# Kernel optimization log

Measured on AMD Instinct MI355X. Metric: run time of the kernel, lower is better.

The kernel has to match this reference:

```python
import jax, jax.numpy as jnp
import numpy as np

NUM_HEADS = 8
HEAD_DIM = 64  # d_model 512 / 8 heads


def rope(x):
    # x: (B, S, D). Rotary applied over the FULL hidden dim (as in source),
    # with even/odd halves CONCATENATED (not interleaved) on output.
    b, s, d = x.shape
    pos = jnp.arange(s, dtype=jnp.float32)[:, None]                      # (S, 1)
    freqs = jnp.exp(jnp.arange(0, d, 2, dtype=jnp.float32) * (-np.log(10000.0) / d))  # (D/2,)
    ang = pos * freqs                                                     # (S, D/2)
    cos = jnp.cos(ang)[None, :, :]
    sin = jnp.sin(ang)[None, :, :]
    xe = x[..., 0::2]
    xo = x[..., 1::2]
    return jnp.concatenate([xe * cos - xo * sin, xo * cos + xe * sin], axis=-1)


def split_heads(x):
    b, s, d = x.shape
    return x.reshape(b, s, NUM_HEADS, HEAD_DIM).transpose(0, 2, 1, 3)  # (B,H,S,hd)


def setup_inputs() -> dict:
    key = jax.random.key(0)
    ks = jax.random.split(key, 8)
    B, S, D = 2, 2048, 512
    sc = 1.0 / np.sqrt(D)
    return {
        "querys": jax.random.normal(ks[0], (B, S, D), jnp.float32),
        "keys": jax.random.normal(ks[1], (B, S, D), jnp.float32),
        "values": jax.random.normal(ks[2], (B, S, D), jnp.float32),
        "attn_mask": jnp.zeros((B, 1, S, S), jnp.float32),
        "Wq": jax.random.normal(ks[3], (D, D), jnp.float32) * sc,
        "Wk": jax.random.normal(ks[4], (D, D), jnp.float32) * sc,
        "Wv": jax.random.normal(ks[5], (D, D), jnp.float32) * sc,
        "Wo": jax.random.normal(ks[6], (D, D), jnp.float32) * sc,
    }


def reference(querys, keys, values, attn_mask, Wq, Wk, Wv, Wo):
    q = split_heads(rope(querys @ Wq.T))   # (B,H,Sq,hd)
    k = split_heads(rope(keys @ Wk.T))     # (B,H,Sk,hd)
    v = split_heads(values @ Wv.T)         # (B,H,Sk,hd)

    logits = jnp.einsum("bhqd,bhkd->bhqk", q, k)
    # mask added BEFORE scaling, exactly as in the source
    logits = logits + attn_mask[:, :, : q.shape[2], : k.shape[2]] * (-1e9)
    attn_scores = jax.nn.softmax(logits / np.float32(HEAD_DIM) ** 0.5, axis=-1)

    embeds = jnp.einsum("bhqk,bhkd->bhqd", attn_scores, v)
    b, h, s, hd = embeds.shape
    embeds = embeds.transpose(0, 2, 1, 3).reshape(b, s, h * hd) @ Wo.T
    return embeds, attn_scores
```

## Files before the change

### kernel.cpp

```cpp
#include <hip/hip_runtime.h>
#include <hip/hip_fp16.h>

typedef _Float16 f16x8 __attribute__((ext_vector_type(8)));
typedef _Float16 f16x4 __attribute__((ext_vector_type(4)));
typedef float f32x16 __attribute__((ext_vector_type(16)));
typedef float f32x4 __attribute__((ext_vector_type(4)));

#define LOG2E 1.44269504088896340736f
#define QSCALE 0.18033688011112042f
#define MASKC 1.8033688e8f

typedef __attribute__((address_space(1))) const unsigned char gl_byte;
typedef __attribute__((address_space(3))) unsigned char lds_byte;

#define GLOAD_LDS16(g, l) \
  __builtin_amdgcn_global_load_lds((const gl_byte*)(g), (lds_byte*)(l), 16, 0, 0)

static __device__ __forceinline__ f32x16 zero16() {
  f32x16 z;
#pragma unroll
  for (int i = 0; i < 16; ++i) z[i] = 0.0f;
  return z;
}

static __device__ __forceinline__ unsigned pkh(float a, float b) {
  union { _Float16 h[2]; unsigned u; } t;
  t.h[0] = (_Float16)a; t.h[1] = (_Float16)b;
  return t.u;
}

static __device__ __forceinline__ void swap32(unsigned x, unsigned y, int hi,
                                              unsigned& a, unsigned& c) {
  unsigned py = (unsigned)__shfl_xor((int)y, 32);
  unsigned px = (unsigned)__shfl_xor((int)x, 32);
  a = hi ? py : x;
  c = hi ? y : px;
}

static __device__ __forceinline__ void stage_k64(char* dst,
                                                 const _Float16* __restrict__ kr,
                                                 int b, int h, int kb, int tid) {
#pragma unroll
  for (int it = 0; it < 4; ++it) {
    int s = it * 128 + tid;
    int r = s >> 3, c8 = (s & 7) ^ (r & 7);
    const _Float16* g = kr + (size_t)(b * 2048 + kb * 64 + r) * 512 + h * 64 + c8 * 8;
    GLOAD_LDS16(g, dst + (it * 128 + (tid & 64)) * 16);
  }
}

__global__ __launch_bounds__(256) void proj_kernel(
    const float* __restrict__ qin, const float* __restrict__ kin,
    const float* __restrict__ vin, const float* __restrict__ Wq,
    const float* __restrict__ Wk, const float* __restrict__ Wv,
    const float* __restrict__ mask, int* __restrict__ flag,
    _Float16* __restrict__ q_r, _Float16* __restrict__ k_r,
    _Float16* __restrict__ v_t) {
  __shared__ char smem[8192 + 16384];
  const int tid = threadIdx.x;
  const int zz = blockIdx.z;

  if (zz == 3) {
    int bid = blockIdx.y * 4 + blockIdx.x;
    const float4* m4p = (const float4*)mask;
    int base = bid * 8192 + tid;
    bool nz = false;
#pragma unroll 4
    for (int i = 0; i < 32; ++i) {
      float4 v = m4p[base + i * 256];
      nz |= (v.x != 0.f) || (v.y != 0.f) || (v.z != 0.f) || (v.w != 0.f);
    }
    if (__any(nz) && (tid & 63) == 0) atomicOr(flag, 1);
    return;
  }

  const int l = tid & 63, lo = l & 31, hi = l >> 5;
  const int w = tid >> 6, wm = w >> 1, wn = w & 1;
  const int m0 = blockIdx.y * 64, n0 = blockIdx.x * 128;
  const float* A = zz == 0 ? qin : zz == 1 ? kin : vin;
  const float* W = zz == 0 ? Wq : zz == 1 ? Wk : Wv;

  f32x16 acc[2];
  acc[0] = zero16();
  acc[1] = zero16();

  for (int kb = 0; kb < 8; ++kb) {
#pragma unroll
    for (int i = 0; i < 4; ++i) {
      int idx = tid + 256 * i; int r = idx >> 4, c4 = idx & 15;
      float4 v = *(const float4*)(A + (size_t)(m0 + r) * 512 + kb * 64 + c4 * 4);
      uint2 uu; uu.x = pkh(v.x, v.y); uu.y = pkh(v.z, v.w);
      *(uint2*)(smem + ((r * 128 + c4 * 8) ^ ((r & 7) << 4))) = uu;
    }
#pragma unroll
    for (int i = 0; i < 8; ++i) {
      int idx = tid + 256 * i; int r = idx >> 4, c4 = idx & 15;
      float4 v = *(const float4*)(W + (size_t)(n0 + r) * 512 + kb * 64 + c4 * 4);
      uint2 uu; uu.x = pkh(v.x, v.y); uu.y = pkh(v.z, v.w);
      *(uint2*)(smem + 8192 + ((r * 128 + c4 * 8) ^ ((r & 7) << 4))) = uu;
    }
    __syncthreads();
#pragma unroll
    for (int ks = 0; ks < 4; ++ks) {
      int ra = wm * 32 + lo;
      f16x8 a0 = *(const f16x8*)(smem + ((ra * 128 + ks * 32 + hi * 16) ^ ((ra & 7) << 4)));
      int rb0 = wn * 64 + lo, rb1 = rb0 + 32;
      f16x8 b0 = *(const f16x8*)(smem + 8192 + ((rb0 * 128 + ks * 32 + hi * 16) ^ ((rb0 & 7) << 4)));
      f16x8 b1 = *(const f16x8*)(smem + 8192 + ((rb1 * 128 + ks * 32 + hi * 16) ^ ((rb1 & 7) << 4)));
      acc[0] = __builtin_amdgcn_mfma_f32_32x32x16_f16(a0, b0, acc[0], 0, 0, 0);
      acc[1] = __builtin_amdgcn_mfma_f32_32x32x16_f16(a0, b1, acc[1], 0, 0, 0);
    }
    __syncthreads();
  }

  if (zz < 2) {
    _Float16* out = zz ? k_r : q_r;
#pragma unroll
    for (int nt = 0; nt < 2; ++nt) {
      int n = n0 + wn * 64 + nt * 32 + lo;
      int odd = lo & 1;
      int ii = (n >> 1) & 255;
      float fr = exp2f(-(float)ii * 0.05190512648261504f);
#pragma unroll
      for (int r = 0; r < 16; ++r) {
        int m = m0 + wm * 32 + (r & 3) + 8 * ((r >> 2) & 3) + 4 * hi;
        float a = acc[nt][r];
        float bb = __shfl_xor(a, 1);
        float xe = odd ? bb : a, xo = odd ? a : bb;
        float ang = (float)(m & 2047) * fr;
        float sn, cs;
        sincosf(ang, &sn, &cs);
        float res = odd ? (xo * cs + xe * sn) : (xe * cs - xo * sn);
        if (zz == 0) res *= QSCALE;
        out[(size_t)m * 512 + ii + (odd ? 256 : 0)] = (_Float16)res;
      }
    }
  } else {
#pragma unroll
    for (int nt = 0; nt < 2; ++nt) {
      int n = n0 + wn * 64 + nt * 32 + lo;
      int hh = n >> 6, d = n & 63;
#pragma unroll
      for (int a = 0; a < 4; ++a) {
        int m = m0 + wm * 32 + 8 * a + 4 * hi;
        int b_ = m >> 11, s = m & 2047;
        uint2 uu;
        uu.x = pkh(acc[nt][4 * a + 0], acc[nt][4 * a + 1]);
        uu.y = pkh(acc[nt][4 * a + 2], acc[nt][4 * a + 3]);
        *(uint2*)(v_t + (size_t)((b_ * 8 + hh) * 64 + d) * 2048 + s) = uu;
      }
    }
  }
}

__global__ __launch_bounds__(256) void out_gemm(const _Float16* __restrict__ opart,
                                                const float* __restrict__ W,
                                                float* __restrict__ out) {
  __shared__ char smem[8192 + 16384];
  const int tid = threadIdx.x;
  const int l = tid & 63, lo = l & 31, hi = l >> 5;
  const int w = tid >> 6, wm = w >> 1, wn = w & 1;
  const int m0 = blockIdx.y * 64, n0 = blockIdx.x * 128;
  const size_t slab = (size_t)4096 * 512;

  f32x16 acc[2];
  acc[0] = zero16();
  acc[1] = zero16();

  for (int kb = 0; kb < 8; ++kb) {
#pragma unroll
    for (int i = 0; i < 4; ++i) {
      int idx = tid + 256 * i; int r = idx >> 4, c4 = idx & 15;
      size_t off = (size_t)(m0 + r) * 512 + kb * 64 + c4 * 4;
      f16x4 x = *(const f16x4*)(opart + off);
      f16x4 y = *(const f16x4*)(opart + slab + off);
      f16x4 u = *(const f16x4*)(opart + 2 * slab + off);
      f16x4 t = *(const f16x4*)(opart + 3 * slab + off);
      float s0 = (float)x[0] + (float)y[0] + (float)u[0] + (float)t[0];
      float s1 = (float)x[1] + (float)y[1] + (float)u[1] + (float)t[1];
      float s2 = (float)x[2] + (float)y[2] + (float)u[2] + (float)t[2];
      float s3 = (float)x[3] + (float)y[3] + (float)u[3] + (float)t[3];
      uint2 uu; uu.x = pkh(s0, s1); uu.y = pkh(s2, s3);
      *(uint2*)(smem + ((r * 128 + c4 * 8) ^ ((r & 7) << 4))) = uu;
    }
#pragma unroll
    for (int i = 0; i < 8; ++i) {
      int idx = tid + 256 * i; int r = idx >> 4, c4 = idx & 15;
      float4 v = *(const float4*)(W + (size_t)(n0 + r) * 512 + kb * 64 + c4 * 4);
      uint2 uu; uu.x = pkh(v.x, v.y); uu.y = pkh(v.z, v.w);
      *(uint2*)(smem + 8192 + ((r * 128 + c4 * 8) ^ ((r & 7) << 4))) = uu;
    }
    __syncthreads();
#pragma unroll
    for (int ks = 0; ks < 4; ++ks) {
      int ra = wm * 32 + lo;
      f16x8 a0 = *(const f16x8*)(smem + ((ra * 128 + ks * 32 + hi * 16) ^ ((ra & 7) << 4)));
      int rb0 = wn * 64 + lo, rb1 = rb0 + 32;
      f16x8 b0 = *(const f16x8*)(smem + 8192 + ((rb0 * 128 + ks * 32 + hi * 16) ^ ((rb0 & 7) << 4)));
      f16x8 b1 = *(const f16x8*)(smem + 8192 + ((rb1 * 128 + ks * 32 + hi * 16) ^ ((rb1 & 7) << 4)));
      acc[0] = __builtin_amdgcn_mfma_f32_32x32x16_f16(a0, b0, acc[0], 0, 0, 0);
      acc[1] = __builtin_amdgcn_mfma_f32_32x32x16_f16(a0, b1, acc[1], 0, 0, 0);
    }
    __syncthreads();
  }

#pragma unroll
  for (int nt = 0; nt < 2; ++nt) {
    int n = n0 + wn * 64 + nt * 32 + lo;
#pragma unroll
    for (int r = 0; r < 16; ++r) {
      int m = m0 + wm * 32 + (r & 3) + 8 * ((r >> 2) & 3) + 4 * hi;
      out[(size_t)m * 512 + n] = acc[nt][r];
    }
  }
}

__global__ __launch_bounds__(128, 4) void lsum_kernel(
    const _Float16* __restrict__ qr, const _Float16* __restrict__ kr,
    const float* __restrict__ mask, const int* __restrict__ flagp,
    float* __restrict__ lsums) {
  __shared__ char smem[16384];
  const int tid = threadIdx.x;
  const int w = tid >> 6, l = tid & 63, lo = l & 31, hi = l >> 5;
  const int bh = blockIdx.y, b = bh >> 3, h = bh & 7;
  const int q0 = blockIdx.x * 64, z = blockIdx.z;
  const int mflag = *flagp;
  const int qw = q0 + w * 32 + lo;

  f16x8 qf[4];
  {
    const _Float16* qrow = qr + (size_t)(b * 2048 + qw) * 512 + h * 64 + hi * 8;
#pragma unroll
    for (int ks = 0; ks < 4; ++ks) qf[ks] = *(const f16x8*)(qrow + ks * 16);
  }

  const int kb0 = z * 8;
  stage_k64(smem, kr, b, h, kb0, tid);
  __syncthreads();

  float lsum = 0.f;
  for (int t = 0; t < 8; ++t) {
    const int cur = t & 1, kb = kb0 + t;
    if (t < 7) stage_k64(smem + (cur ^ 1) * 8192, kr, b, h, kb + 1, tid);
    char* kbuf = smem + cur * 8192;
#pragma unroll
    for (int ks4 = 0; ks4 < 2; ++ks4) {
      f32x16 acc = zero16();
      int krw = ks4 * 32 + lo;
#pragma unroll
      for (int ks = 0; ks < 4; ++ks) {
        f16x8 kf = *(const f16x8*)(kbuf + ((krw * 128 + ks * 32 + hi * 16) ^ ((krw & 7) << 4)));
        acc = __builtin_amdgcn_mfma_f32_32x32x16_f16(kf, qf[ks], acc, 0, 0, 0);
      }
      if (!mflag) {
#pragma unroll
        for (int r = 0; r < 16; ++r) lsum += exp2f(acc[r]);
      } else {
#pragma unroll
        for (int r = 0; r < 16; ++r) {
          int kg = kb * 64 + ks4 * 32 + (r & 3) + 8 * ((r >> 2) & 3) + 4 * hi;
          float mv = mask[(size_t)(b * 2048 + qw) * 2048 + kg];
          lsum += exp2f(acc[r] - MASKC * mv);
        }
      }
    }
    __syncthreads();
  }
  lsum += __shfl_xor(lsum, 32);
  if (hi == 0) lsums[(size_t)(z * 16 + bh) * 2048 + qw] = lsum;
}

__global__ __launch_bounds__(128, 4) void attn_kernel(
    const _Float16* __restrict__ qr, const _Float16* __restrict__ kr,
    const _Float16* __restrict__ vt, const float* __restrict__ mask,
    const int* __restrict__ flagp, const float* __restrict__ lsums,
    float* __restrict__ scores, _Float16* __restrict__ opart) {
  __shared__ char smem[24576];
  const int tid = threadIdx.x;
  const int w = tid >> 6, l = tid & 63, lo = l & 31, hi = l >> 5;
  const int bh = blockIdx.y, b = bh >> 3, h = bh & 7;
  const int q0 = blockIdx.x * 64, z = blockIdx.z;
  const int mflag = *flagp;
  const int qw = q0 + w * 32 + lo;

  f16x8 qf[4];
  {
    const _Float16* qrow = qr + (size_t)(b * 2048 + qw) * 512 + h * 64 + hi * 8;
#pragma unroll
    for (int ks = 0; ks < 4; ++ks) qf[ks] = *(const f16x8*)(qrow + ks * 16);
  }

  float lsum = 0.f;
#pragma unroll
  for (int zz = 0; zz < 4; ++zz) lsum += lsums[(size_t)(zz * 16 + bh) * 2048 + qw];
  const float linv = -log2f(lsum);

  f32x16 oacc[2];
  oacc[0] = zero16();
  oacc[1] = zero16();
  char* trw = smem + 16384 + (w << 12);
  const _Float16* vbase = vt + (size_t)((b * 8 + h) * 64) * 2048;

  const int kb0 = z * 8;
  stage_k64(smem, kr, b, h, kb0, tid);
  __syncthreads();

  for (int t = 0; t < 8; ++t) {
    const int cur = t & 1, kb = kb0 + t;
    if (t < 7) stage_k64(smem + (cur ^ 1) * 8192, kr, b, h, kb + 1, tid);
    f16x8 vp[8];
#pragma unroll
    for (int f = 0; f < 8; ++f) {
      int ks4 = f >> 2, kb2 = (f >> 1) & 1, dt = f & 1;
      int d = dt * 32 + lo;
      vp[f] = *(const f16x8*)(vbase + (size_t)d * 2048 + kb * 64 + ks4 * 32 + kb2 * 16 + hi * 8);
    }
    char* kbuf = smem + cur * 8192;
#pragma unroll
    for (int ks4 = 0; ks4 < 2; ++ks4) {
      f32x16 acc = zero16();
      int krw = ks4 * 32 + lo;
#pragma unroll
      for (int ks = 0; ks < 4; ++ks) {
        f16x8 kf = *(const f16x8*)(kbuf + ((krw * 128 + ks * 32 + hi * 16) ^ ((krw & 7) << 4)));
        acc = __builtin_amdgcn_mfma_f32_32x32x16_f16(kf, qf[ks], acc, 0, 0, 0);
      }
      float p[16];
      if (!mflag) {
#pragma unroll
        for (int r = 0; r < 16; ++r) p[r] = exp2f(acc[r] + linv);
      } else {
#pragma unroll
        for (int r = 0; r < 16; ++r) {
          int kg = kb * 64 + ks4 * 32 + (r & 3) + 8 * ((r >> 2) & 3) + 4 * hi;
          float mv = mask[(size_t)(b * 2048 + qw) * 2048 + kg];
          p[r] = exp2f(acc[r] - MASKC * mv + linv);
        }
      }
#pragma unroll
      for (int a = 0; a < 4; ++a) {
        int g = ((2 * a + hi) ^ (lo >> 2)) & 7;
        f32x4 v;
        v[0] = p[4 * a + 0]; v[1] = p[4 * a + 1];
        v[2] = p[4 * a + 2]; v[3] = p[4 * a + 3];
        *(f32x4*)(trw + lo * 128 + (g << 4)) = v;
      }
#pragma unroll
      for (int kb2 = 0; kb2 < 2; ++kb2) {
        unsigned X0 = pkh(p[8 * kb2 + 0], p[8 * kb2 + 1]);
        unsigned X1 = pkh(p[8 * kb2 + 2], p[8 * kb2 + 3]);
        unsigned Y0 = pkh(p[8 * kb2 + 4], p[8 * kb2 + 5]);
        unsigned Y1 = pkh(p[8 * kb2 + 6], p[8 * kb2 + 7]);
        unsigned w0, w1, w2, w3;
        swap32(X0, Y0, hi, w0, w2);
        swap32(X1, Y1, hi, w1, w3);
        union { unsigned u[4]; f16x8 v; } pf;
        pf.u[0] = w0; pf.u[1] = w1; pf.u[2] = w2; pf.u[3] = w3;
#pragma unroll
        for (int dt = 0; dt < 2; ++dt)
          oacc[dt] = __builtin_amdgcn_mfma_f32_32x32x16_f16(vp[ks4 * 4 + kb2 * 2 + dt],
                                                            pf.v, oacc[dt], 0, 0, 0);
      }
      float* srow = scores + (size_t)(bh * 2048 + q0 + w * 32) * 2048 + kb * 64 + ks4 * 32;
      {
        int qrd = l >> 3, k4 = l & 7, m4 = (l & 7) << 2;
#pragma unroll
        for (int j = 0; j < 4; ++j) {
          int q = qrd + 8 * j;
          int g = (k4 ^ (q >> 2)) & 7;
          f32x4 o = *(const f32x4*)(trw + q * 128 + (g << 4));
          __builtin_nontemporal_store(o, (f32x4*)(srow + (size_t)q * 2048 + m4));
        }
      }
    }
    __syncthreads();
  }
  _Float16* orow = opart + (size_t)z * 4096 * 512 + (size_t)(b * 2048 + qw) * 512 + h * 64;
#pragma unroll
  for (int dt = 0; dt < 2; ++dt)
#pragma unroll
    for (int a = 0; a < 4; ++a) {
      int d = dt * 32 + 8 * a + 4 * hi;
      uint2 uu;
      uu.x = pkh(oacc[dt][4 * a + 0], oacc[dt][4 * a + 1]);
      uu.y = pkh(oacc[dt][4 * a + 2], oacc[dt][4 * a + 3]);
      *(uint2*)(orow + d) = uu;
    }
}

extern "C" void kernel_launch(void* const* d_in, const int* in_sizes, int n_in,
                              void* d_out, int out_size, void* d_ws, size_t ws_size,
                              hipStream_t stream) {
  const float* querys = (const float*)d_in[0];
  const float* keys   = (const float*)d_in[1];
  const float* values = (const float*)d_in[2];
  const float* mask   = (const float*)d_in[3];
  const float* Wq = (const float*)d_in[4];
  const float* Wk = (const float*)d_in[5];
  const float* Wv = (const float*)d_in[6];
  const float* Wo = (const float*)d_in[7];

  char* ws = (char*)d_ws;
  const size_t MB = 1048576;
  _Float16* q_r   = (_Float16*)(ws + 0 * MB);
  _Float16* k_r   = (_Float16*)(ws + 4 * MB);
  _Float16* v_t   = (_Float16*)(ws + 8 * MB);
  _Float16* opart = (_Float16*)(ws + 12 * MB);
  float*    lsums = (float*)(ws + 28 * MB);
  int*      flag  = (int*)(ws + 29 * MB);

  float* out_sc = (float*)d_out + (size_t)4096 * 512;

  (void)hipMemsetAsync(flag, 0, 4, stream);

  proj_kernel<<<dim3(4, 64, 4), 256, 0, stream>>>(querys, keys, values, Wq, Wk, Wv,
                                                  mask, flag, q_r, k_r, v_t);

  lsum_kernel<<<dim3(32, 16, 4), 128, 0, stream>>>(q_r, k_r, mask, flag, lsums);

  attn_kernel<<<dim3(32, 16, 4), 128, 0, stream>>>(q_r, k_r, v_t, mask, flag, lsums,
                                                   out_sc, opart);

  out_gemm<<<dim3(4, 64), 256, 0, stream>>>(opart, Wo, (float*)d_out);
}
```

Baseline: 182.9 us.

## Fuse lsum and attention passes into one cooperative kernel with grid sync

Merges the separate row-sum kernel and the attention kernel into a single cooperative launch that computes partial softmax denominators, synchronises the whole grid, then computes probabilities, scores and partial outputs. The key range is split into 3 slices instead of 4, so the grid of 1536 blocks stays co-resident, and out_gemm now takes a variable slab count. This removes one kernel launch boundary, and the Q fragments stay in registers across both phases. In exchange it adds a grid-wide barrier, a runtime occupancy query on the host, and less parallelism per block.

```diff
diff --git a/kernel.cpp b/kernel.cpp
--- a/kernel.cpp
+++ b/kernel.cpp
@@ -1,5 +1,8 @@
 #include <hip/hip_runtime.h>
 #include <hip/hip_fp16.h>
+#include <hip/hip_cooperative_groups.h>
+
+namespace cg = cooperative_groups;
 
 typedef _Float16 f16x8 __attribute__((ext_vector_type(8)));
 typedef _Float16 f16x4 __attribute__((ext_vector_type(4)));
@@ -155,7 +158,7 @@
 
 __global__ __launch_bounds__(256) void out_gemm(const _Float16* __restrict__ opart,
                                                 const float* __restrict__ W,
-                                                float* __restrict__ out) {
+                                                float* __restrict__ out, int nslab) {
   __shared__ char smem[8192 + 16384];
   const int tid = threadIdx.x;
   const int l = tid & 63, lo = l & 31, hi = l >> 5;
@@ -172,14 +175,11 @@
     for (int i = 0; i < 4; ++i) {
       int idx = tid + 256 * i; int r = idx >> 4, c4 = idx & 15;
       size_t off = (size_t)(m0 + r) * 512 + kb * 64 + c4 * 4;
-      f16x4 x = *(const f16x4*)(opart + off);
-      f16x4 y = *(const f16x4*)(opart + slab + off);
-      f16x4 u = *(const f16x4*)(opart + 2 * slab + off);
-      f16x4 t = *(const f16x4*)(opart + 3 * slab + off);
-      float s0 = (float)x[0] + (float)y[0] + (float)u[0] + (float)t[0];
-      float s1 = (float)x[1] + (float)y[1] + (float)u[1] + (float)t[1];
-      float s2 = (float)x[2] + (float)y[2] + (float)u[2] + (float)t[2];
-      float s3 = (float)x[3] + (float)y[3] + (float)u[3] + (float)t[3];
+      float s0 = 0.f, s1 = 0.f, s2 = 0.f, s3 = 0.f;
+      for (int zz = 0; zz < nslab; ++zz) {
+        f16x4 x = *(const f16x4*)(opart + zz * slab + off);
+        s0 += (float)x[0]; s1 += (float)x[1]; s2 += (float)x[2]; s3 += (float)x[3];
+      }
       uint2 uu; uu.x = pkh(s0, s1); uu.y = pkh(s2, s3);
       *(uint2*)(smem + ((r * 128 + c4 * 8) ^ ((r & 7) << 4))) = uu;
     }
@@ -213,6 +213,162 @@
       out[(size_t)m * 512 + n] = acc[nt][r];
     }
   }
+}
+
+__global__ __launch_bounds__(128, 4) void fused_attn(
+    const _Float16* __restrict__ qr, const _Float16* __restrict__ kr,
+    const _Float16* __restrict__ vt, const float* __restrict__ mask,
+    const int* __restrict__ flagp, float* __restrict__ lsums,
+    float* __restrict__ scores, _Float16* __restrict__ opart) {
+  __shared__ char smem[24576];
+  const int tid = threadIdx.x;
+  const int w = tid >> 6, l = tid & 63, lo = l & 31, hi = l >> 5;
+  const int bh = blockIdx.y, b = bh >> 3, h = bh & 7;
+  const int q0 = blockIdx.x * 64, z = blockIdx.z;
+  const int mflag = *flagp;
+  const int qw = q0 + w * 32 + lo;
+  const int t0 = (z * 16) / 3, t1 = ((z + 1) * 16) / 3;
+
+  f16x8 qf[4];
+  {
+    const _Float16* qrow = qr + (size_t)(b * 2048 + qw) * 512 + h * 64 + hi * 8;
+#pragma unroll
+    for (int ks = 0; ks < 4; ++ks) qf[ks] = *(const f16x8*)(qrow + ks * 16);
+  }
+
+  {
+    stage_k64(smem, kr, b, h, t0, tid);
+    __syncthreads();
+    float lsum = 0.f;
+    for (int t = t0; t < t1; ++t) {
+      const int cur = (t - t0) & 1;
+      if (t + 1 < t1) stage_k64(smem + (cur ^ 1) * 8192, kr, b, h, t + 1, tid);
+      char* kbuf = smem + cur * 8192;
+#pragma unroll
+      for (int ks4 = 0; ks4 < 2; ++ks4) {
+        f32x16 acc = zero16();
+        int krw = ks4 * 32 + lo;
+#pragma unroll
+        for (int ks = 0; ks < 4; ++ks) {
+          f16x8 kf = *(const f16x8*)(kbuf + ((krw * 128 + ks * 32 + hi * 16) ^ ((krw & 7) << 4)));
+          acc = __builtin_amdgcn_mfma_f32_32x32x16_f16(kf, qf[ks], acc, 0, 0, 0);
+        }
+        if (!mflag) {
+#pragma unroll
+          for (int r = 0; r < 16; ++r) lsum += exp2f(acc[r]);
+        } else {
+#pragma unroll
+          for (int r = 0; r < 16; ++r) {
+            int kg = t * 64 + ks4 * 32 + (r & 3) + 8 * ((r >> 2) & 3) + 4 * hi;
+            float mv = mask[(size_t)(b * 2048 + qw) * 2048 + kg];
+            lsum += exp2f(acc[r] - MASKC * mv);
+          }
+        }
+      }
+      __syncthreads();
+    }
+    lsum += __shfl_xor(lsum, 32);
+    if (hi == 0) lsums[(size_t)(z * 16 + bh) * 2048 + qw] = lsum;
+  }
+
+  __threadfence();
+  cg::this_grid().sync();
+
+  float lsum = 0.f;
+#pragma unroll
+  for (int zz = 0; zz < 3; ++zz) lsum += lsums[(size_t)(zz * 16 + bh) * 2048 + qw];
+  const float linv = -log2f(lsum);
+
+  f32x16 oacc[2];
+  oacc[0] = zero16();
+  oacc[1] = zero16();
+  char* trw = smem + 16384 + (w << 12);
+  const _Float16* vbase = vt + (size_t)((b * 8 + h) * 64) * 2048;
+
+  stage_k64(smem, kr, b, h, t0, tid);
+  __syncthreads();
+
+  for (int t = t0; t < t1; ++t) {
+    const int cur = (t - t0) & 1;
+    if (t + 1 < t1) stage_k64(smem + (cur ^ 1) * 8192, kr, b, h, t + 1, tid);
+    f16x8 vp[8];
+#pragma unroll
+    for (int f = 0; f < 8; ++f) {
+      int ks4 = f >> 2, kb2 = (f >> 1) & 1, dt = f & 1;
+      int d = dt * 32 + lo;
+      vp[f] = *(const f16x8*)(vbase + (size_t)d * 2048 + t * 64 + ks4 * 32 + kb2 * 16 + hi * 8);
+    }
+    char* kbuf = smem + cur * 8192;
+#pragma unroll
+    for (int ks4 = 0; ks4 < 2; ++ks4) {
+      f32x16 acc = zero16();
+      int krw = ks4 * 32 + lo;
+#pragma unroll
+      for (int ks = 0; ks < 4; ++ks) {
+        f16x8 kf = *(const f16x8*)(kbuf + ((krw * 128 + ks * 32 + hi * 16) ^ ((krw & 7) << 4)));
+        acc = __builtin_amdgcn_mfma_f32_32x32x16_f16(kf, qf[ks], acc, 0, 0, 0);
+      }
+      float p[16];
+      if (!mflag) {
+#pragma unroll
+        for (int r = 0; r < 16; ++r) p[r] = exp2f(acc[r] + linv);
+      } else {
+#pragma unroll
+        for (int r = 0; r < 16; ++r) {
+          int kg = t * 64 + ks4 * 32 + (r & 3) + 8 * ((r >> 2) & 3) + 4 * hi;
+          float mv = mask[(size_t)(b * 2048 + qw) * 2048 + kg];
+          p[r] = exp2f(acc[r] - MASKC * mv + linv);
+        }
+      }
+#pragma unroll
+      for (int a = 0; a < 4; ++a) {
+        int g = ((2 * a + hi) ^ (lo >> 2)) & 7;
+        f32x4 v;
+        v[0] = p[4 * a + 0]; v[1] = p[4 * a + 1];
+        v[2] = p[4 * a + 2]; v[3] = p[4 * a + 3];
+        *(f32x4*)(trw + lo * 128 + (g << 4)) = v;
+      }
+#pragma unroll
+      for (int kb2 = 0; kb2 < 2; ++kb2) {
+        unsigned X0 = pkh(p[8 * kb2 + 0], p[8 * kb2 + 1]);
+        unsigned X1 = pkh(p[8 * kb2 + 2], p[8 * kb2 + 3]);
+        unsigned Y0 = pkh(p[8 * kb2 + 4], p[8 * kb2 + 5]);
+        unsigned Y1 = pkh(p[8 * kb2 + 6], p[8 * kb2 + 7]);
+        unsigned w0, w1, w2, w3;
+        swap32(X0, Y0, hi, w0, w2);
+        swap32(X1, Y1, hi, w1, w3);
+        union { unsigned u[4]; f16x8 v; } pf;
+        pf.u[0] = w0; pf.u[1] = w1; pf.u[2] = w2; pf.u[3] = w3;
+#pragma unroll
+        for (int dt = 0; dt < 2; ++dt)
+          oacc[dt] = __builtin_amdgcn_mfma_f32_32x32x16_f16(vp[ks4 * 4 + kb2 * 2 + dt],
+                                                            pf.v, oacc[dt], 0, 0, 0);
+      }
+      float* srow = scores + (size_t)(bh * 2048 + q0 + w * 32) * 2048 + t * 64 + ks4 * 32;
+      {
+        int qrd = l >> 3, k4 = l & 7, m4 = (l & 7) << 2;
+#pragma unroll
+        for (int j = 0; j < 4; ++j) {
+          int q = qrd + 8 * j;
+          int g = (k4 ^ (q >> 2)) & 7;
+          f32x4 o = *(const f32x4*)(trw + q * 128 + (g << 4));
+          __builtin_nontemporal_store(o, (f32x4*)(srow + (size_t)q * 2048 + m4));
+        }
+      }
+    }
+    __syncthreads();
+  }
+  _Float16* orow = opart + (size_t)z * 4096 * 512 + (size_t)(b * 2048 + qw) * 512 + h * 64;
+#pragma unroll
+  for (int dt = 0; dt < 2; ++dt)
+#pragma unroll
+    for (int a = 0; a < 4; ++a) {
+      int d = dt * 32 + 8 * a + 4 * hi;
+      uint2 uu;
+      uu.x = pkh(oacc[dt][4 * a + 0], oacc[dt][4 * a + 1]);
+      uu.y = pkh(oacc[dt][4 * a + 2], oacc[dt][4 * a + 3]);
+      *(uint2*)(orow + d) = uu;
+    }
 }
 
 __global__ __launch_bounds__(128, 4) void lsum_kernel(
@@ -416,10 +572,28 @@
   proj_kernel<<<dim3(4, 64, 4), 256, 0, stream>>>(querys, keys, values, Wq, Wk, Wv,
                                                   mask, flag, q_r, k_r, v_t);
 
+  int maxb = 0;
+  hipError_t qerr = hipOccupancyMaxActiveBlocksPerMultiprocessor(
+      &maxb, fused_attn, 128, 0);
+  bool coop = (qerr == hipSuccess) && (maxb >= 6);
+
+  if (coop) {
+    const _Float16* qr_ = q_r; const _Float16* kr_ = k_r; const _Float16* vt_ = v_t;
+    const float* mask_ = mask; const int* flag_ = flag; float* lsums_ = lsums;
+    float* sc_ = out_sc; _Float16* op_ = opart;
+    void* args[] = {(void*)&qr_, (void*)&kr_, (void*)&vt_, (void*)&mask_,
+                    (void*)&flag_, (void*)&lsums_, (void*)&sc_, (void*)&op_};
+    hipError_t lerr = hipLaunchCooperativeKernel((const void*)fused_attn,
+                                                 dim3(32, 16, 3), dim3(128),
+                                                 args, 0, stream);
+    if (lerr == hipSuccess) {
+      out_gemm<<<dim3(4, 64), 256, 0, stream>>>(opart, Wo, (float*)d_out, 3);
+      return;
+    }
+  }
+
   lsum_kernel<<<dim3(32, 16, 4), 128, 0, stream>>>(q_r, k_r, mask, flag, lsums);
-
   attn_kernel<<<dim3(32, 16, 4), 128, 0, stream>>>(q_r, k_r, v_t, mask, flag, lsums,
                                                    out_sc, opart);
-
-  out_gemm<<<dim3(4, 64), 256, 0, stream>>>(opart, Wo, (float*)d_out);
-}
+  out_gemm<<<dim3(4, 64), 256, 0, stream>>>(opart, Wo, (float*)d_out, 4);
+}
```

New measurement: 197.1 us. 1.08x slower.

## Load K fragments directly from global memory instead of LDS staging

Applied to the files above, without the earlier changes.

Removes the double-buffered global-to-LDS staging of K tiles in both the logsum and attention kernels, having each lane read its K fragments straight from global memory (relying on cache). This drops the per-iteration block barriers and cuts LDS usage in the attention kernel, which could raise occupancy. The cost is that the two waves now fetch K redundantly, and the software prefetch that hid load latency is gone.

```diff
diff --git a/kernel.cpp b/kernel.cpp
--- a/kernel.cpp
+++ b/kernel.cpp
@@ -9,12 +9,6 @@
 #define LOG2E 1.44269504088896340736f
 #define QSCALE 0.18033688011112042f
 #define MASKC 1.8033688e8f
-
-typedef __attribute__((address_space(1))) const unsigned char gl_byte;
-typedef __attribute__((address_space(3))) unsigned char lds_byte;
-
-#define GLOAD_LDS16(g, l) \
-  __builtin_amdgcn_global_load_lds((const gl_byte*)(g), (lds_byte*)(l), 16, 0, 0)
 
 static __device__ __forceinline__ f32x16 zero16() {
   f32x16 z;
@@ -35,18 +29,6 @@
   unsigned px = (unsigned)__shfl_xor((int)x, 32);
   a = hi ? py : x;
   c = hi ? y : px;
-}
-
-static __device__ __forceinline__ void stage_k64(char* dst,
-                                                 const _Float16* __restrict__ kr,
-                                                 int b, int h, int kb, int tid) {
-#pragma unroll
-  for (int it = 0; it < 4; ++it) {
-    int s = it * 128 + tid;
-    int r = s >> 3, c8 = (s & 7) ^ (r & 7);
-    const _Float16* g = kr + (size_t)(b * 2048 + kb * 64 + r) * 512 + h * 64 + c8 * 8;
-    GLOAD_LDS16(g, dst + (it * 128 + (tid & 64)) * 16);
-  }
 }
 
 __global__ __launch_bounds__(256) void proj_kernel(
@@ -219,7 +201,6 @@
     const _Float16* __restrict__ qr, const _Float16* __restrict__ kr,
     const float* __restrict__ mask, const int* __restrict__ flagp,
     float* __restrict__ lsums) {
-  __shared__ char smem[16384];
   const int tid = threadIdx.x;
   const int w = tid >> 6, l = tid & 63, lo = l & 31, hi = l >> 5;
   const int bh = blockIdx.y, b = bh >> 3, h = bh & 7;
@@ -233,23 +214,20 @@
 #pragma unroll
     for (int ks = 0; ks < 4; ++ks) qf[ks] = *(const f16x8*)(qrow + ks * 16);
   }
+  const _Float16* kbase = kr + (size_t)(b * 2048) * 512 + h * 64 + hi * 8;
 
   const int kb0 = z * 8;
-  stage_k64(smem, kr, b, h, kb0, tid);
-  __syncthreads();
-
   float lsum = 0.f;
   for (int t = 0; t < 8; ++t) {
-    const int cur = t & 1, kb = kb0 + t;
-    if (t < 7) stage_k64(smem + (cur ^ 1) * 8192, kr, b, h, kb + 1, tid);
-    char* kbuf = smem + cur * 8192;
+    const int kb = kb0 + t;
 #pragma unroll
     for (int ks4 = 0; ks4 < 2; ++ks4) {
+      int krow = kb * 64 + ks4 * 32 + lo;
+      const _Float16* krow_p = kbase + (size_t)krow * 512;
       f32x16 acc = zero16();
-      int krw = ks4 * 32 + lo;
 #pragma unroll
       for (int ks = 0; ks < 4; ++ks) {
-        f16x8 kf = *(const f16x8*)(kbuf + ((krw * 128 + ks * 32 + hi * 16) ^ ((krw & 7) << 4)));
+        f16x8 kf = *(const f16x8*)(krow_p + ks * 16);
         acc = __builtin_amdgcn_mfma_f32_32x32x16_f16(kf, qf[ks], acc, 0, 0, 0);
       }
       if (!mflag) {
@@ -264,7 +242,6 @@
         }
       }
     }
-    __syncthreads();
   }
   lsum += __shfl_xor(lsum, 32);
   if (hi == 0) lsums[(size_t)(z * 16 + bh) * 2048 + qw] = lsum;
@@ -275,7 +252,7 @@
     const _Float16* __restrict__ vt, const float* __restrict__ mask,
     const int* __restrict__ flagp, const float* __restrict__ lsums,
     float* __restrict__ scores, _Float16* __restrict__ opart) {
-  __shared__ char smem[24576];
+  __shared__ char smem[8192];
   const int tid = threadIdx.x;
   const int w = tid >> 6, l = tid & 63, lo = l & 31, hi = l >> 5;
   const int bh = blockIdx.y, b = bh >> 3, h = bh & 7;
@@ -289,6 +266,7 @@
 #pragma unroll
     for (int ks = 0; ks < 4; ++ks) qf[ks] = *(const f16x8*)(qrow + ks * 16);
   }
+  const _Float16* kbase = kr + (size_t)(b * 2048) * 512 + h * 64 + hi * 8;
 
   float lsum = 0.f;
 #pragma unroll
@@ -298,16 +276,12 @@
   f32x16 oacc[2];
   oacc[0] = zero16();
   oacc[1] = zero16();
-  char* trw = smem + 16384 + (w << 12);
+  char* trw = smem + (w << 12);
   const _Float16* vbase = vt + (size_t)((b * 8 + h) * 64) * 2048;
 
   const int kb0 = z * 8;
-  stage_k64(smem, kr, b, h, kb0, tid);
-  __syncthreads();
-
   for (int t = 0; t < 8; ++t) {
-    const int cur = t & 1, kb = kb0 + t;
-    if (t < 7) stage_k64(smem + (cur ^ 1) * 8192, kr, b, h, kb + 1, tid);
+    const int kb = kb0 + t;
     f16x8 vp[8];
 #pragma unroll
     for (int f = 0; f < 8; ++f) {
@@ -315,14 +289,14 @@
       int d = dt * 32 + lo;
       vp[f] = *(const f16x8*)(vbase + (size_t)d * 2048 + kb * 64 + ks4 * 32 + kb2 * 16 + hi * 8);
     }
-    char* kbuf = smem + cur * 8192;
 #pragma unroll
     for (int ks4 = 0; ks4 < 2; ++ks4) {
+      int krow = kb * 64 + ks4 * 32 + lo;
+      const _Float16* krow_p = kbase + (size_t)krow * 512;
       f32x16 acc = zero16();
-      int krw = ks4 * 32 + lo;
 #pragma unroll
       for (int ks = 0; ks < 4; ++ks) {
-        f16x8 kf = *(const f16x8*)(kbuf + ((krw * 128 + ks * 32 + hi * 16) ^ ((krw & 7) << 4)));
+        f16x8 kf = *(const f16x8*)(krow_p + ks * 16);
         acc = __builtin_amdgcn_mfma_f32_32x32x16_f16(kf, qf[ks], acc, 0, 0, 0);
       }
       float p[16];
@@ -373,7 +347,6 @@
         }
       }
     }
-    __syncthreads();
   }
   _Float16* orow = opart + (size_t)z * 4096 * 512 + (size_t)(b * 2048 + qw) * 512 + h * 64;
 #pragma unroll
```

After: 206.4 us. 12.8% more time.
